# Kernel optimization log

Hardware: AMD Instinct MI355X
Metric: run time of the kernel (lower is better)

## Reference

```python
import jax, jax.numpy as jnp
import numpy as np

NB, NA, NC, NH, NW = 128, 5, 80, 28, 28
NT = 50
ANCHORS = jnp.array([2.8, 4.8, 5.1, 10.2, 6.4, 16.3, 9.2, 19.8, 14.1, 23.7], dtype=jnp.float32)
ANCHOR_W = ANCHORS[0::2]  # [NA]
ANCHOR_H = ANCHORS[1::2]
OBJECT_SCALE = 5.0
NOOBJECT_SCALE = 1.0
CLASS_SCALE = 1.0
COORD_SCALE = 1.0
SIL_THRESH = 0.6


def iou_cxcywh(b1, b2):
    # center-format IoU, matches bbox_ious(x1y1x2y2=False); inputs broadcastable (...,4)
    x1, y1, w1, h1 = b1[..., 0], b1[..., 1], b1[..., 2], b1[..., 3]
    x2, y2, w2, h2 = b2[..., 0], b2[..., 1], b2[..., 2], b2[..., 3]
    mx = jnp.minimum(x1 - w1 / 2, x2 - w2 / 2)
    Mx = jnp.maximum(x1 + w1 / 2, x2 + w2 / 2)
    my = jnp.minimum(y1 - h1 / 2, y2 - h2 / 2)
    My = jnp.maximum(y1 + h1 / 2, y2 + h2 / 2)
    cw = w1 + w2 - (Mx - mx)
    ch = h1 + h2 - (My - my)
    inter = jnp.where((cw > 0) & (ch > 0), cw * ch, 0.0)
    union = w1 * h1 + w2 * h2 - inter
    return inter / union


def build_targets(pred_boxes, target):
    # pred_boxes: [NB, NA, NH, NW, 4] grid-unit cxcywh (already detached)
    tgt = target.reshape(NB, NT, 5)
    gcls = tgt[..., 0]
    gx = tgt[..., 1] * NW
    gy = tgt[..., 2] * NH
    gw = tgt[..., 3] * NW
    gh = tgt[..., 4] * NH
    gt_boxes = jnp.stack([gx, gy, gw, gh], -1)  # [NB, NT, 4]

    # silence mask: any-GT IoU > thresh -> conf_mask 0, else noobject_scale
    pb = pred_boxes.reshape(NB, NA * NH * NW, 4)
    ious = iou_cxcywh(pb[:, :, None, :], gt_boxes[:, None, :, :])  # [NB, nAnchors, NT]
    max_iou = jnp.max(ious, axis=2)
    conf_mask0 = jnp.where(max_iou > SIL_THRESH, 0.0, NOOBJECT_SCALE).reshape(NB, NA, NH, NW)

    # best anchor per GT by wh-only IoU at origin
    z_na = jnp.zeros((NA,), jnp.float32)
    anc = jnp.stack([z_na, z_na, ANCHOR_W, ANCHOR_H], -1)  # [NA,4]
    zg = jnp.zeros_like(gw)
    gt_wh = jnp.stack([zg, zg, gw, gh], -1)  # [NB,NT,4]
    a_iou = iou_cxcywh(gt_wh[:, :, None, :], anc[None, None, :, :])  # [NB,NT,NA]
    best_n = jnp.argmax(a_iou, axis=2)  # [NB,NT] (first max, matches strict > loop)

    gi = jnp.floor(gx).astype(jnp.int32)
    gj = jnp.floor(gy).astype(jnp.int32)
    flat_idx = ((jnp.arange(NB)[:, None] * NA + best_n) * NH + gj) * NW + gi  # [NB,NT]

    assigned_pred = pred_boxes.reshape(NB * NA * NH * NW, 4)[flat_idx]  # [NB,NT,4]
    iou_gt_pred = iou_cxcywh(gt_boxes, assigned_pred)  # [NB,NT]
    aw = ANCHOR_W[best_n]
    ah = ANCHOR_H[best_n]

    idx = flat_idx.reshape(-1)
    grid0 = jnp.zeros((NB * NA * NH * NW,), jnp.float32)

    def sc(init_flat, v):
        return init_flat.at[idx].set(v.reshape(-1)).reshape(NB, NA, NH, NW)

    ones = jnp.ones((NB, NT), jnp.float32)
    coord_mask = sc(grid0, ones)
    cls_mask = sc(grid0, ones)
    conf_mask = sc(conf_mask0.reshape(-1), jnp.full((NB, NT), OBJECT_SCALE, jnp.float32))
    tx = sc(grid0, gx - gi.astype(jnp.float32))
    ty = sc(grid0, gy - gj.astype(jnp.float32))
    tw = sc(grid0, jnp.log(gw / aw))
    th = sc(grid0, jnp.log(gh / ah))
    tconf = sc(grid0, iou_gt_pred)
    tcls = sc(grid0, gcls)
    return coord_mask, conf_mask, cls_mask, tx, ty, tw, th, tconf, tcls


def _smooth_l1_sum(a, b):
    d = a - b
    ad = jnp.abs(d)
    return jnp.sum(jnp.where(ad < 1.0, 0.5 * d * d, ad - 0.5))


def _forward(output, target):
    out = output.reshape(NB, NA, 5 + NC, NH, NW)
    x = jax.nn.sigmoid(out[:, :, 0])
    y = jax.nn.sigmoid(out[:, :, 1])
    w = out[:, :, 2]
    h = out[:, :, 3]
    conf = jax.nn.sigmoid(out[:, :, 4])
    cls_logits = jnp.transpose(out[:, :, 5:], (0, 1, 3, 4, 2))  # [NB,NA,NH,NW,NC]

    gx = jnp.arange(NW, dtype=jnp.float32)[None, None, None, :]
    gy = jnp.arange(NH, dtype=jnp.float32)[None, None, :, None]
    sg = jax.lax.stop_gradient
    px = sg(x) + gx
    py = sg(y) + gy
    pw = jnp.exp(sg(w)) * ANCHOR_W[None, :, None, None]
    ph = jnp.exp(sg(h)) * ANCHOR_H[None, :, None, None]
    pred_boxes = jnp.stack([px, py, pw, ph], -1)  # [NB,NA,NH,NW,4]

    bt = jax.lax.stop_gradient(build_targets(pred_boxes, target))
    coord_mask, conf_mask, cls_mask, tx, ty, tw, th, tconf, tcls = bt
    conf_mask = jnp.sqrt(conf_mask)

    loss_x = COORD_SCALE * _smooth_l1_sum(x * coord_mask, tx * coord_mask) / 2.0
    loss_y = COORD_SCALE * _smooth_l1_sum(y * coord_mask, ty * coord_mask) / 2.0
    loss_w = COORD_SCALE * _smooth_l1_sum(w * coord_mask, tw * coord_mask) / 2.0
    loss_h = COORD_SCALE * _smooth_l1_sum(h * coord_mask, th * coord_mask) / 2.0
    loss_conf = jnp.sum((conf * conf_mask - tconf * conf_mask) ** 2) / 2.0

    # focal loss (gamma=2, alpha=1, sum reduction) over cells with cls_mask==1
    logp = jax.nn.log_softmax(cls_logits, axis=-1)
    logp_t = jnp.take_along_axis(logp, tcls[..., None].astype(jnp.int32), axis=-1)[..., 0]
    p_t = jnp.exp(logp_t)
    focal = -((1.0 - p_t) ** 2) * logp_t
    loss_cls = CLASS_SCALE * jnp.sum(cls_mask * focal)

    return loss_x + loss_y + loss_w + loss_h + loss_conf + loss_cls


def setup_inputs() -> dict:
    key = jax.random.key(0)
    k1, k2, k3 = jax.random.split(key, 3)
    output = jax.random.normal(k1, (NB, NA * (5 + NC), NH, NW), dtype=jnp.float32)
    u = jax.random.uniform(k2, (NB, NT, 4), dtype=jnp.float32)
    xy = 0.1 + 0.8 * u[..., :2]   # x in (0.1,0.9) -> never 0, no early break
    wh = 0.05 + 0.45 * u[..., 2:]
    cls_id = jax.random.randint(k3, (NB, NT, 1), 0, NC).astype(jnp.float32)
    target = jnp.concatenate([cls_id, xy, wh], axis=-1).reshape(NB, NT * 5)
    return {"output": output, "target": target}


def reference(output, target):
    return _forward(output, target)
```

## Files before the change

kernel.cpp:

```cpp
#include <hip/hip_runtime.h>
#include <math.h>

#define NBB 128
#define NAA 5
#define NCC 80
#define NHH 28
#define NWW 28
#define NTT 50
#define CH  85
#define HW  784
#define CELLS 3920

__constant__ float c_AW[5] = {2.8f, 5.1f, 6.4f, 9.2f, 14.1f};
__constant__ float c_AH[5] = {4.8f, 10.2f, 16.3f, 19.8f, 23.7f};

__device__ __forceinline__ float sigmoidf_(float x) {
    return 1.0f / (1.0f + __expf(-x));
}

__device__ __forceinline__ float smooth_l1(float d) {
    float ad = fabsf(d);
    return (ad < 1.0f) ? 0.5f * d * d : ad - 0.5f;
}

__global__ __launch_bounds__(256) void region_loss_fused(
    const float* __restrict__ out, const float* __restrict__ tgt,
    float* __restrict__ d_out)
{
    __shared__ float L2[NTT], R2[NTT], T2[NTT], B2[NTT], AR[NTT];
    __shared__ int   rCell[NTT];
    __shared__ float rTc[NTT], rTx[NTT], rTy[NTT], rTw[NTT], rTh[NTT];
    __shared__ int   rCls[NTT];
    __shared__ unsigned char rActive[NTT];
    __shared__ float red[256];
    __shared__ float waveS[4];

    const int b   = blockIdx.y;
    const int tid = threadIdx.x;

    if (tid < NTT) {
        const float* tp = tgt + b * NTT * 5 + tid * 5;
        float cls = tp[0];
        float gx = tp[1] * NWW;
        float gy = tp[2] * NHH;
        float gw = tp[3] * NWW;
        float gh = tp[4] * NHH;
        float ga = gw * gh;

        L2[tid] = gx - gw * 0.5f;
        R2[tid] = gx + gw * 0.5f;
        T2[tid] = gy - gh * 0.5f;
        B2[tid] = gy + gh * 0.5f;
        AR[tid] = ga;

        int best = 0; float bestI = -1.0f;
        #pragma unroll
        for (int a = 0; a < 5; ++a) {
            float inter = fminf(gw, c_AW[a]) * fminf(gh, c_AH[a]);
            float uni   = ga + c_AW[a] * c_AH[a] - inter;
            float iou   = inter / uni;
            if (iou > bestI) { bestI = iou; best = a; }
        }
        int gi = (int)floorf(gx);
        int gj = (int)floorf(gy);
        int cell = (best * NHH + gj) * NWW + gi;

        const float* op = out + ((size_t)(b * NAA + best) * CH) * HW + gj * NWW + gi;
        float px = sigmoidf_(op[0])      + (float)gi;
        float py = sigmoidf_(op[HW])     + (float)gj;
        float pw = __expf(op[2 * HW]) * c_AW[best];
        float ph = __expf(op[3 * HW]) * c_AH[best];

        float mx = fminf(px - pw * 0.5f, gx - gw * 0.5f);
        float Mx = fmaxf(px + pw * 0.5f, gx + gw * 0.5f);
        float my = fminf(py - ph * 0.5f, gy - gh * 0.5f);
        float My = fmaxf(py + ph * 0.5f, gy + gh * 0.5f);
        float cw  = pw + gw - (Mx - mx);
        float chh = ph + gh - (My - my);
        float inter = (cw > 0.f && chh > 0.f) ? cw * chh : 0.f;
        float uni   = pw * ph + ga - inter;

        rCell[tid] = cell;
        rTc[tid]   = inter / uni;
        rTx[tid]   = gx - (float)gi;
        rTy[tid]   = gy - (float)gj;
        rTw[tid]   = __logf(gw / c_AW[best]);
        rTh[tid]   = __logf(gh / c_AH[best]);
        rCls[tid]  = (int)cls;
    }
    __syncthreads();

    if (tid < NTT) {
        int cell = rCell[tid];
        unsigned char active = 1;
        for (int t2 = tid + 1; t2 < NTT; ++t2)
            if (rCell[t2] == cell) active = 0;
        rActive[tid] = active;
    }

    const int cell = blockIdx.x * 256 + tid;
    float term = 0.0f;

    if (cell < CELLS) {
        int a  = cell / HW;
        int hw = cell - a * HW;
        int wi = hw % NWW;
        int hj = hw / NWW;
        const float* op = out + ((size_t)(b * NAA + a) * CH) * HW + hw;

        float px   = sigmoidf_(op[0])  + (float)wi;
        float py   = sigmoidf_(op[HW]) + (float)hj;
        float pw   = __expf(op[2 * HW]) * c_AW[a];
        float ph   = __expf(op[3 * HW]) * c_AH[a];
        float conf = sigmoidf_(op[4 * HW]);

        float l1 = px - pw * 0.5f, r1 = px + pw * 0.5f;
        float t1 = py - ph * 0.5f, b1 = py + ph * 0.5f;
        float a1 = pw * ph;

        bool flag = false;
        #pragma unroll 5
        for (int j = 0; j < NTT; ++j) {
            float cw  = fminf(r1, R2[j]) - fmaxf(l1, L2[j]);
            float chh = fminf(b1, B2[j]) - fmaxf(t1, T2[j]);
            float inter = (cw > 0.f && chh > 0.f) ? cw * chh : 0.f;
            flag = flag || (inter * 1.6f > 0.6f * (a1 + AR[j]));
        }

        bool assigned = false; float tc = 0.f;
        for (int j = 0; j < NTT; ++j) {
            if (rCell[j] == cell) { assigned = true; tc = rTc[j]; }
        }

        if (assigned) { float d = conf - tc; term = 2.5f * d * d; }
        else if (!flag) { term = 0.5f * conf * conf; }
    }

    const int wave = tid >> 6;
    const int lane = tid & 63;
    const int j    = blockIdx.x * 4 + wave;
    float contrib = 0.0f;

    __syncthreads();

    if (j < NTT && rActive[j]) {
        int rc = rCell[j];
        int a  = rc / HW;
        int hw = rc - a * HW;
        const float* op = out + ((size_t)(b * NAA + a) * CH) * HW + hw;

        float l0 = op[(5 + lane) * HW];
        float l1 = (lane < 16) ? op[(5 + 64 + lane) * HW] : -INFINITY;

        float m = fmaxf(l0, l1);
        for (int o = 32; o >= 1; o >>= 1) m = fmaxf(m, __shfl_xor(m, o));
        float s = __expf(l0 - m) + ((lane < 16) ? __expf(l1 - m) : 0.0f);
        for (int o = 32; o >= 1; o >>= 1) s += __shfl_xor(s, o);

        int t = rCls[j];
        float lt = (t < 64) ? __shfl(l0, t) : __shfl(l1, t - 64);
        float logpt = lt - m - __logf(s);
        float pt = __expf(logpt);
        float focal = -(1.0f - pt) * (1.0f - pt) * logpt;

        if (lane == 0) {
            float x = sigmoidf_(op[0]);
            float y = sigmoidf_(op[HW]);
            float w = op[2 * HW];
            float h = op[3 * HW];
            contrib = focal +
                      0.5f * (smooth_l1(x - rTx[j]) + smooth_l1(y - rTy[j]) +
                              smooth_l1(w - rTw[j]) + smooth_l1(h - rTh[j]));
        }
    }
    if (lane == 0) waveS[wave] = contrib;

    red[tid] = term;
    __syncthreads();
    for (int s = 128; s > 0; s >>= 1) {
        if (tid < s) red[tid] += red[tid + s];
        __syncthreads();
    }
    if (tid == 0)
        atomicAdd(d_out, red[0] + waveS[0] + waveS[1] + waveS[2] + waveS[3]);
}

extern "C" void kernel_launch(void* const* d_in, const int* in_sizes, int n_in,
                              void* d_out, int out_size, void* d_ws, size_t ws_size,
                              hipStream_t stream) {
    const float* out_p = (const float*)d_in[0];
    const float* tgt_p = (const float*)d_in[1];
    float* loss = (float*)d_out;

    hipMemsetAsync(loss, 0, (size_t)out_size * sizeof(float), stream);

    region_loss_fused<<<dim3(16, NBB), dim3(256), 0, stream>>>(
        out_p, tgt_p, loss);
}
```

Before: 237.4 us.

## Use 1024-thread blocks, merge GT loops, pack shared data, wave-shuffle reduction

Blocks grow from 256 to 1024 threads, so each batch gets 4 blocks instead of 16. That cuts how often the per-GT setup (target loads, anchor matching, pred gather) is repeated per batch. The silence IoU loop and the assignment-lookup loop are merged into one pass over shared float4/float2 packed GT data, and the IoU threshold test is rewritten algebraically to avoid a multiply. The shared-memory tree reduction is replaced by wave shuffles plus a 16-entry sum. The larger blocks may reduce occupancy flexibility, and the last block per batch leaves many threads idle (3920 cells over 4096 threads).

```diff
diff --git a/kernel.cpp b/kernel.cpp
--- a/kernel.cpp
+++ b/kernel.cpp
@@ -23,17 +23,18 @@
     return (ad < 1.0f) ? 0.5f * d * d : ad - 0.5f;
 }
 
-__global__ __launch_bounds__(256) void region_loss_fused(
+__global__ __launch_bounds__(1024) void region_loss_fused(
     const float* __restrict__ out, const float* __restrict__ tgt,
     float* __restrict__ d_out)
 {
-    __shared__ float L2[NTT], R2[NTT], T2[NTT], B2[NTT], AR[NTT];
-    __shared__ int   rCell[NTT];
-    __shared__ float rTc[NTT], rTx[NTT], rTy[NTT], rTw[NTT], rTh[NTT];
-    __shared__ int   rCls[NTT];
+    __shared__ float4 boxS[NTT];
+    __shared__ float  s6[NTT];
+    __shared__ float2 ctS[NTT];
+    __shared__ int    rCell[NTT];
+    __shared__ float  rTx[NTT], rTy[NTT], rTw[NTT], rTh[NTT];
+    __shared__ int    rCls[NTT];
     __shared__ unsigned char rActive[NTT];
-    __shared__ float red[256];
-    __shared__ float waveS[4];
+    __shared__ float  wred[16];
 
     const int b   = blockIdx.y;
     const int tid = threadIdx.x;
@@ -47,11 +48,9 @@
         float gh = tp[4] * NHH;
         float ga = gw * gh;
 
-        L2[tid] = gx - gw * 0.5f;
-        R2[tid] = gx + gw * 0.5f;
-        T2[tid] = gy - gh * 0.5f;
-        B2[tid] = gy + gh * 0.5f;
-        AR[tid] = ga;
+        boxS[tid] = make_float4(gx - gw * 0.5f, gx + gw * 0.5f,
+                                gy - gh * 0.5f, gy + gh * 0.5f);
+        s6[tid] = 0.375f * ga;
 
         int best = 0; float bestI = -1.0f;
         #pragma unroll
@@ -81,7 +80,7 @@
         float uni   = pw * ph + ga - inter;
 
         rCell[tid] = cell;
-        rTc[tid]   = inter / uni;
+        ctS[tid]   = make_float2(__int_as_float(cell), inter / uni);
         rTx[tid]   = gx - (float)gi;
         rTy[tid]   = gy - (float)gj;
         rTw[tid]   = __logf(gw / c_AW[best]);
@@ -98,7 +97,7 @@
         rActive[tid] = active;
     }
 
-    const int cell = blockIdx.x * 256 + tid;
+    const int cell = blockIdx.x * 1024 + tid;
     float term = 0.0f;
 
     if (cell < CELLS) {
@@ -116,20 +115,21 @@
 
         float l1 = px - pw * 0.5f, r1 = px + pw * 0.5f;
         float t1 = py - ph * 0.5f, b1 = py + ph * 0.5f;
-        float a1 = pw * ph;
-
-        bool flag = false;
+        float c1 = 0.375f * (pw * ph);
+
+        bool flag = false, assigned = false;
+        float tc = 0.f;
         #pragma unroll 5
         for (int j = 0; j < NTT; ++j) {
-            float cw  = fminf(r1, R2[j]) - fmaxf(l1, L2[j]);
-            float chh = fminf(b1, B2[j]) - fmaxf(t1, T2[j]);
-            float inter = (cw > 0.f && chh > 0.f) ? cw * chh : 0.f;
-            flag = flag || (inter * 1.6f > 0.6f * (a1 + AR[j]));
-        }
-
-        bool assigned = false; float tc = 0.f;
-        for (int j = 0; j < NTT; ++j) {
-            if (rCell[j] == cell) { assigned = true; tc = rTc[j]; }
+            float4 bx = boxS[j];
+            float cw  = fminf(r1, bx.y) - fmaxf(l1, bx.x);
+            float ch2 = fminf(b1, bx.w) - fmaxf(t1, bx.z);
+            float inter = fmaxf(cw, 0.f) * fmaxf(ch2, 0.f);
+            flag = flag || (inter > c1 + s6[j]);
+            float2 c2 = ctS[j];
+            bool hit = (__float_as_int(c2.x) == cell);
+            assigned = assigned || hit;
+            tc = hit ? c2.y : tc;
         }
 
         if (assigned) { float d = conf - tc; term = 2.5f * d * d; }
@@ -138,7 +138,7 @@
 
     const int wave = tid >> 6;
     const int lane = tid & 63;
-    const int j    = blockIdx.x * 4 + wave;
+    const int j    = blockIdx.x * 16 + wave;
     float contrib = 0.0f;
 
     __syncthreads();
@@ -149,16 +149,16 @@
         int hw = rc - a * HW;
         const float* op = out + ((size_t)(b * NAA + a) * CH) * HW + hw;
 
-        float l0 = op[(5 + lane) * HW];
-        float l1 = (lane < 16) ? op[(5 + 64 + lane) * HW] : -INFINITY;
-
-        float m = fmaxf(l0, l1);
+        float l0  = op[(5 + lane) * HW];
+        float l1c = (lane < 16) ? op[(5 + 64 + lane) * HW] : -INFINITY;
+
+        float m = fmaxf(l0, l1c);
         for (int o = 32; o >= 1; o >>= 1) m = fmaxf(m, __shfl_xor(m, o));
-        float s = __expf(l0 - m) + ((lane < 16) ? __expf(l1 - m) : 0.0f);
+        float s = __expf(l0 - m) + ((lane < 16) ? __expf(l1c - m) : 0.0f);
         for (int o = 32; o >= 1; o >>= 1) s += __shfl_xor(s, o);
 
         int t = rCls[j];
-        float lt = (t < 64) ? __shfl(l0, t) : __shfl(l1, t - 64);
+        float lt = (t < 64) ? __shfl(l0, t) : __shfl(l1c, t - 64);
         float logpt = lt - m - __logf(s);
         float pt = __expf(logpt);
         float focal = -(1.0f - pt) * (1.0f - pt) * logpt;
@@ -173,16 +173,18 @@
                               smooth_l1(w - rTw[j]) + smooth_l1(h - rTh[j]));
         }
     }
-    if (lane == 0) waveS[wave] = contrib;
-
-    red[tid] = term;
+
+    float v = term + ((lane == 0) ? contrib : 0.0f);
+    #pragma unroll
+    for (int o = 32; o >= 1; o >>= 1) v += __shfl_xor(v, o);
+    if (lane == 0) wred[wave] = v;
     __syncthreads();
-    for (int s = 128; s > 0; s >>= 1) {
-        if (tid < s) red[tid] += red[tid + s];
-        __syncthreads();
-    }
-    if (tid == 0)
-        atomicAdd(d_out, red[0] + waveS[0] + waveS[1] + waveS[2] + waveS[3]);
+    if (tid == 0) {
+        float s = 0.0f;
+        #pragma unroll
+        for (int w2 = 0; w2 < 16; ++w2) s += wred[w2];
+        atomicAdd(d_out, s);
+    }
 }
 
 extern "C" void kernel_launch(void* const* d_in, const int* in_sizes, int n_in,
@@ -194,6 +196,6 @@
 
     hipMemsetAsync(loss, 0, (size_t)out_size * sizeof(float), stream);
 
-    region_loss_fused<<<dim3(16, NBB), dim3(256), 0, stream>>>(
+    region_loss_fused<<<dim3(4, NBB), dim3(1024), 0, stream>>>(
         out_p, tgt_p, loss);
 }
```

After: 222.1 us. 6.5% less time.
